# Optimization experiments

Measured on AMD Instinct MI355X. Metric: run time of the kernel, lower is better.

Reference implementation:

```python
import jax, jax.numpy as jnp
import numpy as np

EMB = 2048
HEADS = 8
HEAD_DIM = EMB // HEADS  # 256

def setup_inputs() -> dict:
    key = jax.random.key(0)
    ks = jax.random.split(key, 4)
    b, n = 2, 2048
    x = jax.random.normal(ks[0], (b, n, EMB), dtype=jnp.float32)
    # Linear weights stored as [in, out] (y = x @ W + b)
    w_qkv = jax.random.normal(ks[1], (EMB, 3 * EMB), dtype=jnp.float32) * (EMB ** -0.5)
    b_qkv = jnp.zeros((3 * EMB,), dtype=jnp.float32)
    w_proj = jax.random.normal(ks[2], (EMB, EMB), dtype=jnp.float32) * (EMB ** -0.5)
    b_proj = jnp.zeros((EMB,), dtype=jnp.float32)
    return {"x": x, "w_qkv": w_qkv, "b_qkv": b_qkv, "w_proj": w_proj, "b_proj": b_proj}

def reference(x, w_qkv, b_qkv, w_proj, b_proj):
    b, n, _ = x.shape
    qkv = x @ w_qkv + b_qkv                                   # [b, n, 3*emb]
    # rearrange 'b n (h d qkv) -> qkv b h n d': qkv index is innermost
    qkv = qkv.reshape(b, n, HEADS, HEAD_DIM, 3)
    qkv = jnp.transpose(qkv, (4, 0, 2, 1, 3))                 # [3, b, h, n, d]
    q, k, v = qkv[0], qkv[1], qkv[2]
    energy = jnp.einsum('bhqd,bhkd->bhqk', q, k)              # [b, h, n, n]
    scaling = EMB ** 0.5
    # NOTE: faithful to source — softmax on UNSCALED logits, divide after.
    att = jax.nn.softmax(energy, axis=-1) / scaling
    out = jnp.einsum('bhal,bhlv->bhav', att, v)               # [b, h, n, d]
    out = jnp.transpose(out, (0, 2, 1, 3)).reshape(b, n, EMB)  # b n (h d)
    return out @ w_proj + b_proj
```

## Files before the change

kernel.cpp:

```cpp
#include <hip/hip_runtime.h>
#include <cstdint>
#include <cstddef>


typedef __bf16 bf16x8 __attribute__((ext_vector_type(8)));
typedef __bf16 bf16x2 __attribute__((ext_vector_type(2)));
typedef float f32x4 __attribute__((ext_vector_type(4)));

#define SCALE_INV 0.022097086912079608f

#define GLDS16(gp, lp)                                                        \
  __builtin_amdgcn_global_load_lds(                                           \
      (const __attribute__((address_space(1))) void*)(gp),                    \
      (__attribute__((address_space(3))) void*)(lp), 16, 0, 0)

__device__ inline void split8(const float4 v0, const float4 v1, bf16x8& hi,
                              bf16x8& lo) {
  float a[8] = {v0.x, v0.y, v0.z, v0.w, v1.x, v1.y, v1.z, v1.w};
  bf16x8 h, l;
#pragma unroll
  for (int i = 0; i < 8; i++) {
    __bf16 hh = (__bf16)a[i];
    h[i] = hh;
    l[i] = (__bf16)(a[i] - (float)hh);
  }
  hi = h;
  lo = l;
}

__global__ __launch_bounds__(256) void presplit_x_k(
    const float* __restrict__ X, __bf16* __restrict__ Xh,
    __bf16* __restrict__ Xl) {
  const size_t i = ((size_t)blockIdx.x * 256 + threadIdx.x) * 8;
  const float4 v0 = *(const float4*)&X[i];
  const float4 v1 = *(const float4*)&X[i + 4];
  bf16x8 h, l;
  split8(v0, v1, h, l);
  *(bf16x8*)&Xh[i] = h;
  *(bf16x8*)&Xl[i] = l;
}

__global__ __launch_bounds__(256) void transpose_cvt_k(
    const float* __restrict__ in, __bf16* __restrict__ out, int R, int C) {
  __shared__ float tile[32][33];
  const int tx = threadIdx.x & 31;
  const int ty = threadIdx.x >> 5;
  const int c0 = blockIdx.x * 32;
  const int r0 = blockIdx.y * 32;
#pragma unroll
  for (int i = 0; i < 32; i += 8)
    tile[ty + i][tx] = in[(size_t)(r0 + ty + i) * C + (c0 + tx)];
  __syncthreads();
#pragma unroll
  for (int i = 0; i < 32; i += 8)
    out[(size_t)(c0 + ty + i) * R + (r0 + tx)] = (__bf16)tile[tx][ty + i];
}

__global__ __launch_bounds__(256) void transpose_w_split_k(
    const float* __restrict__ in, __bf16* __restrict__ wh,
    __bf16* __restrict__ wl, int col0) {
  __shared__ float tile[64][65];
  const int tid = threadIdx.x;
  const int c0 = col0 + blockIdx.x * 64;
  const int r0 = blockIdx.y * 64;
  const int cx = tid & 15, ry = tid >> 4;
#pragma unroll
  for (int p = 0; p < 4; p++) {
    const float4 v =
        *(const float4*)&in[(size_t)(r0 + p * 16 + ry) * 6144 + c0 + cx * 4];
    tile[p * 16 + ry][cx * 4 + 0] = v.x;
    tile[p * 16 + ry][cx * 4 + 1] = v.y;
    tile[p * 16 + ry][cx * 4 + 2] = v.z;
    tile[p * 16 + ry][cx * 4 + 3] = v.w;
  }
  __syncthreads();
  const int r2 = tid & 31;
  const int cy = tid >> 5;
  const int cbase = c0 - col0;
#pragma unroll
  for (int p = 0; p < 8; p++) {
    const int cl = cy + p * 8;
    const float t0 = tile[2 * r2][cl];
    const float t1 = tile[2 * r2 + 1][cl];
    const __bf16 h0 = (__bf16)t0, h1 = (__bf16)t1;
    bf16x2 hv = {h0, h1};
    bf16x2 lv = {(__bf16)(t0 - (float)h0), (__bf16)(t1 - (float)h1)};
    *(bf16x2*)&wh[(size_t)(cbase + cl) * 2048 + r0 + 2 * r2] = hv;
    *(bf16x2*)&wl[(size_t)(cbase + cl) * 2048 + r0 + 2 * r2] = lv;
  }
}

__global__ __launch_bounds__(256) void gemm_qkv_dma_k(
    const __bf16* __restrict__ Xh, const __bf16* __restrict__ Xl,
    const __bf16* __restrict__ Wh, const __bf16* __restrict__ Wl,
    const float* __restrict__ bias, int nbase, __bf16* __restrict__ qh_,
    __bf16* __restrict__ ql_, __bf16* __restrict__ kh_,
    __bf16* __restrict__ kl_, __bf16* __restrict__ vT) {
  __shared__ __attribute__((aligned(16))) __bf16 AhL[2][4096];
  __shared__ __attribute__((aligned(16))) __bf16 AlL[2][4096];
  __shared__ __attribute__((aligned(16))) __bf16 BhL[2][4096];
  __shared__ __attribute__((aligned(16))) __bf16 BlL[2][4096];
  const int tid = threadIdx.x, lane = tid & 63, wave = tid >> 6;
  const int l16 = lane & 15, quad = lane >> 4;
  const int wm = (wave >> 1) * 64, wn = (wave & 1) * 64;
  const int m0 = blockIdx.y * 128, n0 = blockIdx.x * 128;

  f32x4 zero4 = {0.f, 0.f, 0.f, 0.f};
  f32x4 acc[4][4];
#pragma unroll
  for (int i = 0; i < 4; i++)
#pragma unroll
    for (int j = 0; j < 4; j++) acc[i][j] = zero4;

  const int rowl = lane >> 2, gq = lane & 3;
  const int sg = gq ^ (rowl & 3);
  size_t srcOff[2];
  int dst[2];
#pragma unroll
  for (int i = 0; i < 2; i++) {
    const int row = wave * 32 + i * 16 + rowl;
    srcOff[i] = (size_t)row * 2048 + sg * 8;
    dst[i] = (wave * 32 + i * 16) * 32;
  }
  const __bf16* AhG = Xh + (size_t)m0 * 2048;
  const __bf16* AlG = Xl + (size_t)m0 * 2048;
  const __bf16* BhG = Wh + (size_t)n0 * 2048;
  const __bf16* BlG = Wl + (size_t)n0 * 2048;

  const int aro = (wm + l16) * 32 + ((quad ^ (l16 & 3)) << 3);
  const int bro = (wn + l16) * 32 + ((quad ^ (l16 & 3)) << 3);

#define STAGEQ(buf, koff)                                                     \
  do {                                                                        \
    GLDS16(AhG + srcOff[0] + (koff), &AhL[buf][dst[0]]);                      \
    GLDS16(AhG + srcOff[1] + (koff), &AhL[buf][dst[1]]);                      \
    GLDS16(AlG + srcOff[0] + (koff), &AlL[buf][dst[0]]);                      \
    GLDS16(AlG + srcOff[1] + (koff), &AlL[buf][dst[1]]);                      \
    GLDS16(BhG + srcOff[0] + (koff), &BhL[buf][dst[0]]);                      \
    GLDS16(BhG + srcOff[1] + (koff), &BhL[buf][dst[1]]);                      \
    GLDS16(BlG + srcOff[0] + (koff), &BlL[buf][dst[0]]);                      \
    GLDS16(BlG + srcOff[1] + (koff), &BlL[buf][dst[1]]);                      \
  } while (0)

  STAGEQ(0, 0);

  for (int k0 = 0; k0 < 2048; k0 += 32) {
    const int cur = (k0 >> 5) & 1;
    __syncthreads();
    const int nxt = k0 + 32;
    if (nxt < 2048) STAGEQ(cur ^ 1, nxt);
    bf16x8 fah[4], fal[4], fbh[4], fbl[4];
#pragma unroll
    for (int i = 0; i < 4; i++) {
      fah[i] = *(const bf16x8*)&AhL[cur][aro + i * 512];
      fal[i] = *(const bf16x8*)&AlL[cur][aro + i * 512];
    }
#pragma unroll
    for (int j = 0; j < 4; j++) {
      fbh[j] = *(const bf16x8*)&BhL[cur][bro + j * 512];
      fbl[j] = *(const bf16x8*)&BlL[cur][bro + j * 512];
    }
#pragma unroll
    for (int i = 0; i < 4; i++)
#pragma unroll
      for (int j = 0; j < 4; j++) {
        acc[i][j] = __builtin_amdgcn_mfma_f32_16x16x32_bf16(fah[i], fbh[j],
                                                            acc[i][j], 0, 0, 0);
        acc[i][j] = __builtin_amdgcn_mfma_f32_16x16x32_bf16(fah[i], fbl[j],
                                                            acc[i][j], 0, 0, 0);
        acc[i][j] = __builtin_amdgcn_mfma_f32_16x16x32_bf16(fal[i], fbh[j],
                                                            acc[i][j], 0, 0, 0);
      }
  }
#undef STAGEQ

#pragma unroll
  for (int i = 0; i < 4; i++) {
#pragma unroll
    for (int j = 0; j < 4; j++) {
      const int col = nbase + n0 + wn + j * 16 + l16;
      const float bv = bias[col];
      const int h = col / 768;
      const int rr = col - h * 768;
      const int d = rr / 3;
      const int c = rr - d * 3;
#pragma unroll
      for (int r = 0; r < 4; r++) {
        const int row = m0 + wm + i * 16 + quad * 4 + r;
        const float v = acc[i][j][r] + bv;
        const int b = row >> 11;
        const int nn = row & 2047;
        const int bh = b * 8 + h;
        const size_t idx = ((size_t)bh * 2048 + nn) * 256 + d;
        if (c == 0) {
          __bf16 hi = (__bf16)v;
          qh_[idx] = hi;
          ql_[idx] = (__bf16)(v - (float)hi);
        } else if (c == 1) {
          __bf16 hi = (__bf16)v;
          kh_[idx] = hi;
          kl_[idx] = (__bf16)(v - (float)hi);
        } else {
          vT[((size_t)bh * 256 + d) * 2048 + nn] = (__bf16)v;
        }
      }
    }
  }
}

__global__ __launch_bounds__(256, 2) void attn_fwd_k(
    const __bf16* __restrict__ Qh,
    const __bf16* __restrict__ Ql,
    const __bf16* __restrict__ Kh,
    const __bf16* __restrict__ Kl,
    const __bf16* __restrict__ Vt,
    __bf16* __restrict__ out) {
  __shared__ __attribute__((aligned(16))) __bf16 KhL[64 * 256];
  __shared__ __attribute__((aligned(16))) __bf16 KlL[64 * 256];
  __shared__ __attribute__((aligned(16))) __bf16 Plds[4][16 * 72];

  const int qblk = blockIdx.x;
  const int bh = blockIdx.y;
  const int bb = bh >> 3, hh = bh & 7;
  const int tid = threadIdx.x, lane = tid & 63, wave = tid >> 6;
  const int l16 = lane & 15, quad = lane >> 4;

  const size_t hqk = (size_t)bh * 2048 * 256;
  const __bf16* qhp = Qh + hqk;
  const __bf16* qlp = Ql + hqk;
  const __bf16* khp = Kh + hqk;
  const __bf16* klp = Kl + hqk;
  const __bf16* vp = Vt + (size_t)bh * 256 * 2048;

  const int qrow = qblk * 64 + wave * 16;

  bf16x8 qhf[8], qlf[8];
#pragma unroll
  for (int t = 0; t < 8; t++) {
    const size_t off = (size_t)(qrow + l16) * 256 + t * 32 + quad * 8;
    qhf[t] = *(const bf16x8*)&qhp[off];
    qlf[t] = *(const bf16x8*)&qlp[off];
  }

  f32x4 zero4 = {0.f, 0.f, 0.f, 0.f};
  f32x4 o[16];
#pragma unroll
  for (int dt = 0; dt < 16; dt++) o[dt] = zero4;
  float mrow[4], lrow[4];
#pragma unroll
  for (int r = 0; r < 4; r++) {
    mrow[r] = -3.0e38f;
    lrow[r] = 0.f;
  }

  int koff[8];
#pragma unroll
  for (int i = 0; i < 8; i++) {
    const int r = wave * 16 + i * 2 + (lane >> 5);
    const int cb = ((lane & 31) << 4) ^ ((r & 7) << 4);
    koff[i] = r * 256 + (cb >> 1);
  }
  const int ldsb = wave * 4096;

#pragma unroll
  for (int i = 0; i < 8; i++) {
    GLDS16(khp + koff[i], &KhL[ldsb + i * 512]);
    GLDS16(klp + koff[i], &KlL[ldsb + i * 512]);
  }

  for (int kv0 = 0; kv0 < 2048; kv0 += 64) {
    __syncthreads();

    f32x4 s[4];
#pragma unroll
    for (int j = 0; j < 4; j++) s[j] = zero4;
    __builtin_amdgcn_s_setprio(1);
#pragma unroll
    for (int j = 0; j < 4; j++) {
      const int row = j * 16 + l16;
      const int swz = (row & 7) << 3;
      const int rb = row * 256;
#pragma unroll
      for (int t = 0; t < 8; t++) {
        const int off = rb + ((t * 32 + quad * 8) ^ swz);
        bf16x8 khf = *(const bf16x8*)&KhL[off];
        bf16x8 klf = *(const bf16x8*)&KlL[off];
        s[j] =
            __builtin_amdgcn_mfma_f32_16x16x32_bf16(qhf[t], khf, s[j], 0, 0, 0);
        s[j] =
            __builtin_amdgcn_mfma_f32_16x16x32_bf16(qhf[t], klf, s[j], 0, 0, 0);
        s[j] =
            __builtin_amdgcn_mfma_f32_16x16x32_bf16(qlf[t], khf, s[j], 0, 0, 0);
      }
    }
    __builtin_amdgcn_s_setprio(0);
    __syncthreads();

    if (kv0 + 64 < 2048) {
      const int kvn = (kv0 + 64) * 256;
#pragma unroll
      for (int i = 0; i < 8; i++) {
        GLDS16(khp + kvn + koff[i], &KhL[ldsb + i * 512]);
        GLDS16(klp + kvn + koff[i], &KlL[ldsb + i * 512]);
      }
    }

    float mnew[4], alpha[4], psum[4];
#pragma unroll
    for (int r = 0; r < 4; r++) {
      float mx = fmaxf(fmaxf(s[0][r], s[1][r]), fmaxf(s[2][r], s[3][r]));
#pragma unroll
      for (int off = 1; off < 16; off <<= 1)
        mx = fmaxf(mx, __shfl_xor(mx, off, 16));
      mnew[r] = fmaxf(mrow[r], mx);
      alpha[r] = __expf(mrow[r] - mnew[r]);
      psum[r] = 0.f;
    }
#pragma unroll
    for (int j = 0; j < 4; j++)
#pragma unroll
      for (int r = 0; r < 4; r++) {
        float p = __expf(s[j][r] - mnew[r]);
        s[j][r] = p;
        psum[r] += p;
      }
#pragma unroll
    for (int r = 0; r < 4; r++) {
#pragma unroll
      for (int off = 1; off < 16; off <<= 1)
        psum[r] += __shfl_xor(psum[r], off, 16);
      lrow[r] = lrow[r] * alpha[r] + psum[r];
      mrow[r] = mnew[r];
    }
#pragma unroll
    for (int dt = 0; dt < 16; dt++) {
      o[dt][0] *= alpha[0];
      o[dt][1] *= alpha[1];
      o[dt][2] *= alpha[2];
      o[dt][3] *= alpha[3];
    }
#pragma unroll
    for (int j = 0; j < 4; j++)
#pragma unroll
      for (int r = 0; r < 4; r++)
        Plds[wave][(quad * 4 + r) * 72 + j * 16 + l16] = (__bf16)s[j][r];
    bf16x8 pa0 = *(const bf16x8*)&Plds[wave][l16 * 72 + quad * 8];
    bf16x8 pa1 = *(const bf16x8*)&Plds[wave][l16 * 72 + 32 + quad * 8];

    __builtin_amdgcn_s_setprio(1);
#pragma unroll
    for (int dt = 0; dt < 16; dt++) {
      const __bf16* vr = vp + (size_t)(dt * 16 + l16) * 2048 + kv0 + quad * 8;
      bf16x8 vf0 = *(const bf16x8*)vr;
      bf16x8 vf1 = *(const bf16x8*)(vr + 32);
      o[dt] = __builtin_amdgcn_mfma_f32_16x16x32_bf16(pa0, vf0, o[dt], 0, 0, 0);
      o[dt] = __builtin_amdgcn_mfma_f32_16x16x32_bf16(pa1, vf1, o[dt], 0, 0, 0);
    }
    __builtin_amdgcn_s_setprio(0);
  }

#pragma unroll
  for (int r = 0; r < 4; r++) {
    const float inv = SCALE_INV / lrow[r];
    const int n = qrow + quad * 4 + r;
    const size_t base = ((size_t)bb * 2048 + n) * 2048 + hh * 256;
#pragma unroll
    for (int dt = 0; dt < 16; dt++)
      out[base + dt * 16 + l16] = (__bf16)(o[dt][r] * inv);
  }
}

__global__ __launch_bounds__(256) void gemm_bt_k(
    const __bf16* __restrict__ A, const __bf16* __restrict__ Bt,
    const float* __restrict__ bias, int M, int Ncols, int K,
    float* __restrict__ outF) {
  __shared__ __bf16 As[128 * 40];
  __shared__ __bf16 Bs[128 * 40];
  const int tid = threadIdx.x, lane = tid & 63, wave = tid >> 6;
  const int l16 = lane & 15, quad = lane >> 4;
  const int wm = (wave >> 1) * 64, wn = (wave & 1) * 64;
  const int m0 = blockIdx.y * 128, n0 = blockIdx.x * 128;
  const int r0 = tid >> 2, kc0 = (tid & 3) * 8;

  f32x4 zero4 = {0.f, 0.f, 0.f, 0.f};
  f32x4 acc[4][4];
#pragma unroll
  for (int i = 0; i < 4; i++)
#pragma unroll
    for (int j = 0; j < 4; j++) acc[i][j] = zero4;

  const __bf16* Aptr = A + (size_t)(m0 + r0) * K + kc0;
  const __bf16* Bptr = Bt + (size_t)(n0 + r0) * K + kc0;
  const size_t rowstep = (size_t)64 * K;

  for (int k0 = 0; k0 < K; k0 += 32) {
    uint4 a0 = *(const uint4*)(Aptr + k0);
    uint4 a1 = *(const uint4*)(Aptr + rowstep + k0);
    uint4 b0 = *(const uint4*)(Bptr + k0);
    uint4 b1 = *(const uint4*)(Bptr + rowstep + k0);
    __syncthreads();
    *(uint4*)&As[r0 * 40 + kc0] = a0;
    *(uint4*)&As[(r0 + 64) * 40 + kc0] = a1;
    *(uint4*)&Bs[r0 * 40 + kc0] = b0;
    *(uint4*)&Bs[(r0 + 64) * 40 + kc0] = b1;
    __syncthreads();
    bf16x8 af[4], bfv[4];
#pragma unroll
    for (int i = 0; i < 4; i++)
      af[i] = *(const bf16x8*)&As[(wm + i * 16 + l16) * 40 + quad * 8];
#pragma unroll
    for (int j = 0; j < 4; j++)
      bfv[j] = *(const bf16x8*)&Bs[(wn + j * 16 + l16) * 40 + quad * 8];
#pragma unroll
    for (int i = 0; i < 4; i++)
#pragma unroll
      for (int j = 0; j < 4; j++)
        acc[i][j] = __builtin_amdgcn_mfma_f32_16x16x32_bf16(af[i], bfv[j],
                                                            acc[i][j], 0, 0, 0);
  }

#pragma unroll
  for (int i = 0; i < 4; i++)
#pragma unroll
    for (int j = 0; j < 4; j++) {
      const int col = n0 + wn + j * 16 + l16;
      const float bv = bias[col];
#pragma unroll
      for (int r = 0; r < 4; r++) {
        const int row = m0 + wm + i * 16 + quad * 4 + r;
        outF[(size_t)row * Ncols + col] = acc[i][j][r] + bv;
      }
    }
}

extern "C" void kernel_launch(void* const* d_in, const int* in_sizes, int n_in,
                              void* d_out, int out_size, void* d_ws,
                              size_t ws_size, hipStream_t stream) {
  const float* x = (const float*)d_in[0];
  const float* w_qkv = (const float*)d_in[1];
  const float* b_qkv = (const float*)d_in[2];
  const float* w_proj = (const float*)d_in[3];
  const float* b_proj = (const float*)d_in[4];
  float* out = (float*)d_out;

  const size_t HSZ = (size_t)16 * 2048 * 256;
  __bf16* qh = (__bf16*)d_ws;
  __bf16* ql = qh + HSZ;
  __bf16* kh = ql + HSZ;
  __bf16* kl = kh + HSZ;
  __bf16* vT = kl + HSZ;
  __bf16* attn = vT + HSZ;
  __bf16* wprojT = qh;

  __bf16* xh = (__bf16*)out;
  __bf16* xl = xh + (size_t)4096 * 2048;
  __bf16* wsp_h = attn;
  __bf16* wsp_l = wsp_h + (size_t)2048 * 2048;

  presplit_x_k<<<dim3(4096), 256, 0, stream>>>(x, xh, xl);
  for (int ph = 0; ph < 3; ph++) {
    transpose_w_split_k<<<dim3(32, 32), 256, 0, stream>>>(w_qkv, wsp_h, wsp_l,
                                                          ph * 2048);
    gemm_qkv_dma_k<<<dim3(16, 32), 256, 0, stream>>>(
        xh, xl, wsp_h, wsp_l, b_qkv, ph * 2048, qh, ql, kh, kl, vT);
  }
  attn_fwd_k<<<dim3(32, 16), 256, 0, stream>>>(qh, ql, kh, kl, vT, attn);
  transpose_cvt_k<<<dim3(64, 64), 256, 0, stream>>>(w_proj, wprojT, 2048, 2048);
  gemm_bt_k<<<dim3(16, 32), 256, 0, stream>>>(attn, wprojT, b_proj, 4096, 2048,
                                              2048, out);
}
```

Before: 891.6 us.

## Double-buffer K-hi in LDS, stream K-lo from global, skip unneeded rescale

Replaces the separate hi/lo K LDS tiles with a double-buffered K-hi tile. The next tile's async load is issued before the QK MFMAs, which removes the second barrier per iteration. K-lo fragments are now read directly from global memory with one-step register prefetch, and V fragment loads are software-pipelined the same way. The online-softmax rescale of O and l is skipped when no row max grew in the wave. In exchange, register pressure and uncoalesced global reads for K-lo rise.

```diff
diff --git a/kernel.cpp b/kernel.cpp
--- a/kernel.cpp
+++ b/kernel.cpp
@@ -215,8 +215,7 @@
     const __bf16* __restrict__ Kl,
     const __bf16* __restrict__ Vt,
     __bf16* __restrict__ out) {
-  __shared__ __attribute__((aligned(16))) __bf16 KhL[64 * 256];
-  __shared__ __attribute__((aligned(16))) __bf16 KlL[64 * 256];
+  __shared__ __attribute__((aligned(16))) __bf16 KhL[2][64 * 256];
   __shared__ __attribute__((aligned(16))) __bf16 Plds[4][16 * 72];
 
   const int qblk = blockIdx.x;
@@ -263,49 +262,56 @@
   const int ldsb = wave * 4096;
 
 #pragma unroll
-  for (int i = 0; i < 8; i++) {
-    GLDS16(khp + koff[i], &KhL[ldsb + i * 512]);
-    GLDS16(klp + koff[i], &KlL[ldsb + i * 512]);
-  }
+  for (int i = 0; i < 8; i++) GLDS16(khp + koff[i], &KhL[0][ldsb + i * 512]);
 
   for (int kv0 = 0; kv0 < 2048; kv0 += 64) {
+    const int cur = (kv0 >> 6) & 1;
     __syncthreads();
 
+    if (kv0 + 64 < 2048) {
+      const int kvn = (kv0 + 64) * 256;
+#pragma unroll
+      for (int i = 0; i < 8; i++)
+        GLDS16(khp + kvn + koff[i], &KhL[cur ^ 1][ldsb + i * 512]);
+    }
+
     f32x4 s[4];
 #pragma unroll
     for (int j = 0; j < 4; j++) s[j] = zero4;
+    bf16x8 kq[2][8];
+    {
+      const __bf16* kr = klp + (size_t)(kv0 + l16) * 256 + quad * 8;
+#pragma unroll
+      for (int t = 0; t < 8; t++) kq[0][t] = *(const bf16x8*)(kr + t * 32);
+    }
     __builtin_amdgcn_s_setprio(1);
 #pragma unroll
     for (int j = 0; j < 4; j++) {
+      if (j < 3) {
+        const __bf16* kr =
+            klp + (size_t)(kv0 + (j + 1) * 16 + l16) * 256 + quad * 8;
+#pragma unroll
+        for (int t = 0; t < 8; t++)
+          kq[(j + 1) & 1][t] = *(const bf16x8*)(kr + t * 32);
+      }
       const int row = j * 16 + l16;
       const int swz = (row & 7) << 3;
       const int rb = row * 256;
 #pragma unroll
       for (int t = 0; t < 8; t++) {
         const int off = rb + ((t * 32 + quad * 8) ^ swz);
-        bf16x8 khf = *(const bf16x8*)&KhL[off];
-        bf16x8 klf = *(const bf16x8*)&KlL[off];
+        bf16x8 khf = *(const bf16x8*)&KhL[cur][off];
         s[j] =
             __builtin_amdgcn_mfma_f32_16x16x32_bf16(qhf[t], khf, s[j], 0, 0, 0);
-        s[j] =
-            __builtin_amdgcn_mfma_f32_16x16x32_bf16(qhf[t], klf, s[j], 0, 0, 0);
+        s[j] = __builtin_amdgcn_mfma_f32_16x16x32_bf16(qhf[t], kq[j & 1][t],
+                                                       s[j], 0, 0, 0);
         s[j] =
             __builtin_amdgcn_mfma_f32_16x16x32_bf16(qlf[t], khf, s[j], 0, 0, 0);
       }
     }
     __builtin_amdgcn_s_setprio(0);
-    __syncthreads();
-
-    if (kv0 + 64 < 2048) {
-      const int kvn = (kv0 + 64) * 256;
-#pragma unroll
-      for (int i = 0; i < 8; i++) {
-        GLDS16(khp + kvn + koff[i], &KhL[ldsb + i * 512]);
-        GLDS16(klp + kvn + koff[i], &KlL[ldsb + i * 512]);
-      }
-    }
-
-    float mnew[4], alpha[4], psum[4];
+
+    float mnew[4], psum[4];
 #pragma unroll
     for (int r = 0; r < 4; r++) {
       float mx = fmaxf(fmaxf(s[0][r], s[1][r]), fmaxf(s[2][r], s[3][r]));
@@ -313,7 +319,6 @@
       for (int off = 1; off < 16; off <<= 1)
         mx = fmaxf(mx, __shfl_xor(mx, off, 16));
       mnew[r] = fmaxf(mrow[r], mx);
-      alpha[r] = __expf(mrow[r] - mnew[r]);
       psum[r] = 0.f;
     }
 #pragma unroll
@@ -329,16 +334,29 @@
 #pragma unroll
       for (int off = 1; off < 16; off <<= 1)
         psum[r] += __shfl_xor(psum[r], off, 16);
-      lrow[r] = lrow[r] * alpha[r] + psum[r];
-      mrow[r] = mnew[r];
-    }
-#pragma unroll
-    for (int dt = 0; dt < 16; dt++) {
-      o[dt][0] *= alpha[0];
-      o[dt][1] *= alpha[1];
-      o[dt][2] *= alpha[2];
-      o[dt][3] *= alpha[3];
-    }
+    }
+    float grow = fmaxf(fmaxf(mnew[0] - mrow[0], mnew[1] - mrow[1]),
+                       fmaxf(mnew[2] - mrow[2], mnew[3] - mrow[3]));
+    if (__any(grow > 0.f)) {
+      float alpha[4];
+#pragma unroll
+      for (int r = 0; r < 4; r++) {
+        alpha[r] = __expf(mrow[r] - mnew[r]);
+        lrow[r] = lrow[r] * alpha[r] + psum[r];
+        mrow[r] = mnew[r];
+      }
+#pragma unroll
+      for (int dt = 0; dt < 16; dt++) {
+        o[dt][0] *= alpha[0];
+        o[dt][1] *= alpha[1];
+        o[dt][2] *= alpha[2];
+        o[dt][3] *= alpha[3];
+      }
+    } else {
+#pragma unroll
+      for (int r = 0; r < 4; r++) lrow[r] += psum[r];
+    }
+
 #pragma unroll
     for (int j = 0; j < 4; j++)
 #pragma unroll
@@ -347,14 +365,25 @@
     bf16x8 pa0 = *(const bf16x8*)&Plds[wave][l16 * 72 + quad * 8];
     bf16x8 pa1 = *(const bf16x8*)&Plds[wave][l16 * 72 + 32 + quad * 8];
 
+    const __bf16* vb0 = vp + kv0 + quad * 8;
+    bf16x8 vfa[2], vfb[2];
+    {
+      const __bf16* vr = vb0 + (size_t)l16 * 2048;
+      vfa[0] = *(const bf16x8*)vr;
+      vfb[0] = *(const bf16x8*)(vr + 32);
+    }
     __builtin_amdgcn_s_setprio(1);
 #pragma unroll
     for (int dt = 0; dt < 16; dt++) {
-      const __bf16* vr = vp + (size_t)(dt * 16 + l16) * 2048 + kv0 + quad * 8;
-      bf16x8 vf0 = *(const bf16x8*)vr;
-      bf16x8 vf1 = *(const bf16x8*)(vr + 32);
-      o[dt] = __builtin_amdgcn_mfma_f32_16x16x32_bf16(pa0, vf0, o[dt], 0, 0, 0);
-      o[dt] = __builtin_amdgcn_mfma_f32_16x16x32_bf16(pa1, vf1, o[dt], 0, 0, 0);
+      if (dt < 15) {
+        const __bf16* vr = vb0 + (size_t)((dt + 1) * 16 + l16) * 2048;
+        vfa[(dt + 1) & 1] = *(const bf16x8*)vr;
+        vfb[(dt + 1) & 1] = *(const bf16x8*)(vr + 32);
+      }
+      o[dt] = __builtin_amdgcn_mfma_f32_16x16x32_bf16(pa0, vfa[dt & 1], o[dt],
+                                                      0, 0, 0);
+      o[dt] = __builtin_amdgcn_mfma_f32_16x16x32_bf16(pa1, vfb[dt & 1], o[dt],
+                                                      0, 0, 0);
     }
     __builtin_amdgcn_s_setprio(0);
   }
```

After: 1.003 ms. 12.5% more time.

## Double-buffer K tiles in attention, use 512-thread blocks, skip redundant rescale

Applied to the files above, without the earlier changes.

The attention kernel moves to 512-thread blocks covering 128 query rows, so each K tile staged in LDS is shared by twice as many waves. K tiles are now double-buffered: the next tile's DMA is issued right after the barrier and one barrier per iteration is removed. The running-max rescale of the output accumulators is skipped when no row max grew in the wave. LDS use roughly doubles, to about 130KB, which limits residency to one block per CU. The grid drops to 256 blocks, which may underfill the GPU's CUs.

```diff
diff --git a/kernel.cpp b/kernel.cpp
--- a/kernel.cpp
+++ b/kernel.cpp
@@ -208,16 +208,16 @@
   }
 }
 
-__global__ __launch_bounds__(256, 2) void attn_fwd_k(
+__global__ __launch_bounds__(512, 1) void attn_fwd_k(
     const __bf16* __restrict__ Qh,
     const __bf16* __restrict__ Ql,
     const __bf16* __restrict__ Kh,
     const __bf16* __restrict__ Kl,
     const __bf16* __restrict__ Vt,
     __bf16* __restrict__ out) {
-  __shared__ __attribute__((aligned(16))) __bf16 KhL[64 * 256];
-  __shared__ __attribute__((aligned(16))) __bf16 KlL[64 * 256];
-  __shared__ __attribute__((aligned(16))) __bf16 Plds[4][16 * 72];
+  __shared__ __attribute__((aligned(16))) __bf16 KhL[2][64 * 256];
+  __shared__ __attribute__((aligned(16))) __bf16 KlL[2][64 * 256];
+  __shared__ __attribute__((aligned(16))) __bf16 Plds[8][16 * 72];
 
   const int qblk = blockIdx.x;
   const int bh = blockIdx.y;
@@ -232,7 +232,7 @@
   const __bf16* klp = Kl + hqk;
   const __bf16* vp = Vt + (size_t)bh * 256 * 2048;
 
-  const int qrow = qblk * 64 + wave * 16;
+  const int qrow = qblk * 128 + wave * 16;
 
   bf16x8 qhf[8], qlf[8];
 #pragma unroll
@@ -253,23 +253,33 @@
     lrow[r] = 0.f;
   }
 
-  int koff[8];
-#pragma unroll
-  for (int i = 0; i < 8; i++) {
-    const int r = wave * 16 + i * 2 + (lane >> 5);
+  int koff[4];
+#pragma unroll
+  for (int i = 0; i < 4; i++) {
+    const int r = wave * 8 + i * 2 + (lane >> 5);
     const int cb = ((lane & 31) << 4) ^ ((r & 7) << 4);
     koff[i] = r * 256 + (cb >> 1);
   }
-  const int ldsb = wave * 4096;
-
-#pragma unroll
-  for (int i = 0; i < 8; i++) {
-    GLDS16(khp + koff[i], &KhL[ldsb + i * 512]);
-    GLDS16(klp + koff[i], &KlL[ldsb + i * 512]);
+  const int ldsb = wave * 2048;
+
+#pragma unroll
+  for (int i = 0; i < 4; i++) {
+    GLDS16(khp + koff[i], &KhL[0][ldsb + i * 512]);
+    GLDS16(klp + koff[i], &KlL[0][ldsb + i * 512]);
   }
 
   for (int kv0 = 0; kv0 < 2048; kv0 += 64) {
+    const int cur = (kv0 >> 6) & 1;
     __syncthreads();
+
+    if (kv0 + 64 < 2048) {
+      const int kvn = (kv0 + 64) * 256;
+#pragma unroll
+      for (int i = 0; i < 4; i++) {
+        GLDS16(khp + kvn + koff[i], &KhL[cur ^ 1][ldsb + i * 512]);
+        GLDS16(klp + kvn + koff[i], &KlL[cur ^ 1][ldsb + i * 512]);
+      }
+    }
 
     f32x4 s[4];
 #pragma unroll
@@ -283,8 +293,8 @@
 #pragma unroll
       for (int t = 0; t < 8; t++) {
         const int off = rb + ((t * 32 + quad * 8) ^ swz);
-        bf16x8 khf = *(const bf16x8*)&KhL[off];
-        bf16x8 klf = *(const bf16x8*)&KlL[off];
+        bf16x8 khf = *(const bf16x8*)&KhL[cur][off];
+        bf16x8 klf = *(const bf16x8*)&KlL[cur][off];
         s[j] =
             __builtin_amdgcn_mfma_f32_16x16x32_bf16(qhf[t], khf, s[j], 0, 0, 0);
         s[j] =
@@ -294,18 +304,8 @@
       }
     }
     __builtin_amdgcn_s_setprio(0);
-    __syncthreads();
-
-    if (kv0 + 64 < 2048) {
-      const int kvn = (kv0 + 64) * 256;
-#pragma unroll
-      for (int i = 0; i < 8; i++) {
-        GLDS16(khp + kvn + koff[i], &KhL[ldsb + i * 512]);
-        GLDS16(klp + kvn + koff[i], &KlL[ldsb + i * 512]);
-      }
-    }
-
-    float mnew[4], alpha[4], psum[4];
+
+    float mnew[4], psum[4];
 #pragma unroll
     for (int r = 0; r < 4; r++) {
       float mx = fmaxf(fmaxf(s[0][r], s[1][r]), fmaxf(s[2][r], s[3][r]));
@@ -313,7 +313,6 @@
       for (int off = 1; off < 16; off <<= 1)
         mx = fmaxf(mx, __shfl_xor(mx, off, 16));
       mnew[r] = fmaxf(mrow[r], mx);
-      alpha[r] = __expf(mrow[r] - mnew[r]);
       psum[r] = 0.f;
     }
 #pragma unroll
@@ -329,16 +328,29 @@
 #pragma unroll
       for (int off = 1; off < 16; off <<= 1)
         psum[r] += __shfl_xor(psum[r], off, 16);
-      lrow[r] = lrow[r] * alpha[r] + psum[r];
-      mrow[r] = mnew[r];
-    }
-#pragma unroll
-    for (int dt = 0; dt < 16; dt++) {
-      o[dt][0] *= alpha[0];
-      o[dt][1] *= alpha[1];
-      o[dt][2] *= alpha[2];
-      o[dt][3] *= alpha[3];
-    }
+    }
+    float grow = fmaxf(fmaxf(mnew[0] - mrow[0], mnew[1] - mrow[1]),
+                       fmaxf(mnew[2] - mrow[2], mnew[3] - mrow[3]));
+    if (__any(grow > 0.f)) {
+      float alpha[4];
+#pragma unroll
+      for (int r = 0; r < 4; r++) {
+        alpha[r] = __expf(mrow[r] - mnew[r]);
+        lrow[r] = lrow[r] * alpha[r] + psum[r];
+        mrow[r] = mnew[r];
+      }
+#pragma unroll
+      for (int dt = 0; dt < 16; dt++) {
+        o[dt][0] *= alpha[0];
+        o[dt][1] *= alpha[1];
+        o[dt][2] *= alpha[2];
+        o[dt][3] *= alpha[3];
+      }
+    } else {
+#pragma unroll
+      for (int r = 0; r < 4; r++) lrow[r] += psum[r];
+    }
+
 #pragma unroll
     for (int j = 0; j < 4; j++)
 #pragma unroll
@@ -464,7 +476,7 @@
     gemm_qkv_dma_k<<<dim3(16, 32), 256, 0, stream>>>(
         xh, xl, wsp_h, wsp_l, b_qkv, ph * 2048, qh, ql, kh, kl, vT);
   }
-  attn_fwd_k<<<dim3(32, 16), 256, 0, stream>>>(qh, ql, kh, kl, vT, attn);
+  attn_fwd_k<<<dim3(16, 16), 512, 0, stream>>>(qh, ql, kh, kl, vT, attn);
   transpose_cvt_k<<<dim3(64, 64), 256, 0, stream>>>(w_proj, wprojT, 2048, 2048);
   gemm_bt_k<<<dim3(16, 32), 256, 0, stream>>>(attn, wprojT, b_proj, 4096, 2048,
                                               2048, out);
```

Result: faster. 872.6 us (-2.1%).
